# Performance work log

Hardware: AMD Instinct MI355X
Metric: run time of the kernel (lower is better)

Reference implementation:

```python
import jax, jax.numpy as jnp
import numpy as np

B, S, H, NH, HD = 2, 2048, 4096, 32, 128  # batch, seq, hidden, heads, head_dim
THETA = 10000.0
SCALE = HD ** -0.5


def setup_inputs() -> dict:
    key = jax.random.key(0)
    k1, k2, k3 = jax.random.split(key, 3)
    hidden_states = jax.random.normal(k1, (B, S, H), jnp.float32) * 0.02
    w_pack = jax.random.normal(k2, (3 * H, H), jnp.float32) * 0.02  # fused QKV weight
    w_o = jax.random.normal(k3, (H, H), jnp.float32) * 0.02
    positions = jnp.broadcast_to(jnp.arange(S, dtype=jnp.int32), (B, S))
    return {"positions": positions, "hidden_states": hidden_states,
            "w_pack": w_pack, "w_o": w_o}


def _apply_rope(x, positions):
    # x: [B, S, NH, HD]; neox-style (rotate-half) RoPE over full head_dim
    inv_freq = 1.0 / (THETA ** (jnp.arange(0, HD, 2, dtype=jnp.float32) / HD))  # [HD/2]
    ang = positions.astype(jnp.float32)[..., None] * inv_freq  # [B, S, HD/2]
    cos = jnp.cos(ang)[:, :, None, :]  # [B, S, 1, HD/2]
    sin = jnp.sin(ang)[:, :, None, :]
    x1, x2 = x[..., : HD // 2], x[..., HD // 2 :]
    return jnp.concatenate([x1 * cos - x2 * sin, x2 * cos + x1 * sin], axis=-1)


def reference(positions, hidden_states, w_pack, w_o):
    # Fused QKV projection then split (W_pack, bias-free)
    qkv = jnp.einsum('bsh,oh->bso', hidden_states, w_pack)  # [B, S, 3H]
    q, k, v = jnp.split(qkv, 3, axis=-1)
    q = q.reshape(B, S, NH, HD)
    k = k.reshape(B, S, NH, HD)
    v = v.reshape(B, S, NH, HD)
    q = _apply_rope(q, positions)
    k = _apply_rope(k, positions)
    # Causal scaled-dot-product attention
    scores = jnp.einsum('bqhd,bkhd->bhqk', q, k) * SCALE
    causal = jnp.tril(jnp.ones((S, S), dtype=bool))
    scores = jnp.where(causal, scores, jnp.float32(-1e9))
    probs = jax.nn.softmax(scores, axis=-1)
    attn = jnp.einsum('bhqk,bkhd->bqhd', probs, v).reshape(B, S, H)
    return jnp.einsum('bsh,oh->bso', attn, w_o)  # o_proj, bias-free
```

## Files before the change

### kernel.cpp

```cpp
#include <hip/hip_runtime.h>

typedef short short8 __attribute__((ext_vector_type(8)));
typedef float f32x4 __attribute__((ext_vector_type(4)));
typedef unsigned short u16;

static constexpr int BATCH = 2, S = 2048, H = 4096, NHEAD = 32, HDIM = 128;

__device__ __forceinline__ u16 f2b(float f) {
  union { float f; unsigned u; } v; v.f = f;
  return (u16)((v.u + 0x7fffu + ((v.u >> 16) & 1u)) >> 16);
}
__device__ __forceinline__ float b2f(u16 h) {
  union { unsigned u; float f; } v; v.u = ((unsigned)h) << 16;
  return v.f;
}

__device__ __forceinline__ void gl16(const u16* g, u16* l) {
  __builtin_amdgcn_global_load_lds((__attribute__((address_space(1))) void*)g,
                                   (__attribute__((address_space(3))) void*)l,
                                   16, 0, 0);
}

#define MFMA(acc, a, b) \
  acc = __builtin_amdgcn_mfma_f32_16x16x32_bf16(a, b, acc, 0, 0, 0)

__global__ __launch_bounds__(256) void cvt_bf16(const float* __restrict__ in,
                                                u16* __restrict__ out) {
  size_t i = ((size_t)blockIdx.x * 256 + threadIdx.x) * 4;
  float4 v = *(const float4*)(in + i);
  ushort4 o = { f2b(v.x), f2b(v.y), f2b(v.z), f2b(v.w) };
  *(ushort4*)(out + i) = o;
}

template <bool F32OUT>
__global__ __launch_bounds__(512, 2) void gemm256(const u16* __restrict__ A,
                                                  const u16* __restrict__ B,
                                                  void* __restrict__ C,
                                                  int M, int N, int K) {
  __shared__ u16 AL[2][2][128 * 64];
  __shared__ u16 BL[2][2][128 * 64];
  const int nbn = N >> 8;
  const int nwg = (M >> 8) * nbn;
  const int bid = blockIdx.x;
  const int wg = (bid & 7) * (nwg >> 3) + (bid >> 3);
  const int bm = wg / nbn, bn = wg % nbn;
  const int tid = threadIdx.x, lane = tid & 63;
  const int w = tid >> 6, wm = w >> 2, wn = w & 3;
  const int hi = lane >> 4, lo = lane & 15;
  const int nk = K >> 6;

  const u16* Abase = A + (size_t)(bm * 256) * K;
  const u16* Bbase = B + (size_t)(bn * 256) * K;

#define STG_A(buf, half, kt)                                                   \
  { _Pragma("unroll") for (int i = 0; i < 2; ++i) {                            \
      int c = tid + i * 512, r = c >> 3, s = c & 7;                            \
      gl16(Abase + (size_t)((half) * 128 + r) * K + (kt) * 64 +                \
               ((s ^ (r & 7)) * 8),                                            \
           &AL[buf][half][c * 8]);                                             \
    } }
#define STG_B(buf, half, kt)                                                   \
  { _Pragma("unroll") for (int i = 0; i < 2; ++i) {                            \
      int c = tid + i * 512, r = c >> 3, s = c & 7;                            \
      gl16(Bbase + (size_t)((half) * 128 + r) * K + (kt) * 64 +                \
               ((s ^ (r & 7)) * 8),                                            \
           &BL[buf][half][c * 8]);                                             \
    } }
#define PREBAR()                                                               \
  do { __builtin_amdgcn_sched_barrier(0);                                      \
       __builtin_amdgcn_s_barrier(); } while (0)

  f32x4 acc[8][4] = {};

  STG_A(0, 0, 0) STG_A(0, 1, 0) STG_B(0, 0, 0) STG_B(0, 1, 0)
  if (nk > 1) {
    STG_B(1, 0, 1) STG_B(1, 1, 1)
    asm volatile("s_waitcnt vmcnt(4)" ::: "memory");
  } else {
    asm volatile("s_waitcnt vmcnt(0)" ::: "memory");
  }
  __builtin_amdgcn_sched_barrier(0);
  __builtin_amdgcn_s_barrier();

  short8 af[4][2], bf[2][2][2];

  for (int t = 0; t < nk; ++t) {
    const int cur = t & 1;
    const u16* Awave = &AL[cur][wm][0];
    const u16* Bwave = &BL[cur][wn >> 1][0];
    const int lrB = (wn & 1) * 64;

#pragma unroll
    for (int mi = 0; mi < 4; ++mi)
#pragma unroll
      for (int ks = 0; ks < 2; ++ks)
        af[mi][ks] = *(const short8*)&Awave[(mi * 16 + lo) * 64 +
                                            (((ks * 4 + hi) ^ (lo & 7)) * 8)];
#pragma unroll
    for (int ni = 0; ni < 2; ++ni)
#pragma unroll
      for (int ks = 0; ks < 2; ++ks)
        bf[0][ni][ks] = *(const short8*)&Bwave[(lrB + ni * 16 + lo) * 64 +
                                               (((ks * 4 + hi) ^ (lo & 7)) * 8)];
    if (t + 1 < nk) STG_A(cur ^ 1, 0, t + 1)
    PREBAR();
    __builtin_amdgcn_s_setprio(1);
#pragma unroll
    for (int mi = 0; mi < 4; ++mi)
#pragma unroll
      for (int ni = 0; ni < 2; ++ni)
#pragma unroll
        for (int ks = 0; ks < 2; ++ks)
          MFMA(acc[mi][ni], af[mi][ks], bf[0][ni][ks]);
    __builtin_amdgcn_s_setprio(0);
    __builtin_amdgcn_s_barrier();

#pragma unroll
    for (int ni = 0; ni < 2; ++ni)
#pragma unroll
      for (int ks = 0; ks < 2; ++ks)
        bf[1][ni][ks] = *(const short8*)&Bwave[(lrB + 32 + ni * 16 + lo) * 64 +
                                               (((ks * 4 + hi) ^ (lo & 7)) * 8)];
    if (t + 1 < nk) STG_A(cur ^ 1, 1, t + 1)
    PREBAR();
    __builtin_amdgcn_s_setprio(1);
#pragma unroll
    for (int mi = 0; mi < 4; ++mi)
#pragma unroll
      for (int ni = 0; ni < 2; ++ni)
#pragma unroll
        for (int ks = 0; ks < 2; ++ks)
          MFMA(acc[mi][2 + ni], af[mi][ks], bf[1][ni][ks]);
    __builtin_amdgcn_s_setprio(0);
    __builtin_amdgcn_s_barrier();

#pragma unroll
    for (int mi = 0; mi < 4; ++mi)
#pragma unroll
      for (int ks = 0; ks < 2; ++ks)
        af[mi][ks] = *(const short8*)&Awave[((64 + mi * 16 + lo)) * 64 +
                                            (((ks * 4 + hi) ^ (lo & 7)) * 8)];
    if (t + 2 < nk) STG_B(cur, 0, t + 2)
    PREBAR();
    __builtin_amdgcn_s_setprio(1);
#pragma unroll
    for (int mi = 0; mi < 4; ++mi)
#pragma unroll
      for (int ni = 0; ni < 2; ++ni)
#pragma unroll
        for (int ks = 0; ks < 2; ++ks)
          MFMA(acc[4 + mi][2 + ni], af[mi][ks], bf[1][ni][ks]);
    __builtin_amdgcn_s_setprio(0);
    __builtin_amdgcn_s_barrier();

    if (t + 2 < nk) {
      STG_B(cur, 1, t + 2)
      asm volatile("s_waitcnt vmcnt(4)" ::: "memory");
    } else {
      asm volatile("s_waitcnt vmcnt(0)" ::: "memory");
    }
    PREBAR();
    __builtin_amdgcn_s_setprio(1);
#pragma unroll
    for (int mi = 0; mi < 4; ++mi)
#pragma unroll
      for (int ni = 0; ni < 2; ++ni)
#pragma unroll
        for (int ks = 0; ks < 2; ++ks)
          MFMA(acc[4 + mi][ni], af[mi][ks], bf[0][ni][ks]);
    __builtin_amdgcn_s_setprio(0);
    __builtin_amdgcn_s_barrier();
  }

#pragma unroll
  for (int mf = 0; mf < 8; ++mf)
#pragma unroll
    for (int nf = 0; nf < 4; ++nf)
#pragma unroll
      for (int j = 0; j < 4; ++j) {
        size_t idx = (size_t)(bm * 256 + wm * 128 + mf * 16 + hi * 4 + j) * N +
                     bn * 256 + wn * 64 + nf * 16 + lo;
        if (F32OUT) ((float*)C)[idx] = acc[mf][nf][j];
        else        ((u16*)C)[idx]   = f2b(acc[mf][nf][j]);
      }
}

__global__ __launch_bounds__(256) void rope_qk(const u16* __restrict__ qkv,
                                               const int* __restrict__ pos,
                                               u16* __restrict__ qr,
                                               u16* __restrict__ kr) {
  __shared__ float cs[64], sn[64];
  const int bs = blockIdx.x;
  const int b = bs >> 11, s = bs & 2047;
  const int tid = threadIdx.x;
  if (tid < 64) {
    float p = (float)pos[bs];
    float freq = __powf(10000.0f, -(float)tid * (1.0f / 64.0f));
    float a = p * freq;
    sn[tid] = sinf(a);
    cs[tid] = cosf(a);
  }
  __syncthreads();
  const u16* src = qkv + (size_t)bs * 12288;
  for (int i = tid; i < 4096; i += 256) {
    int nh = i >> 7, hd = i & 127, f = hd & 63;
    float c = cs[f], sv = sn[f];
    int oth = (hd < 64) ? i + 64 : i - 64;
    size_t dst = ((size_t)(b * NHEAD + nh) * S + s) * HDIM + hd;
    float x = b2f(src[i]), xo = b2f(src[oth]);
    qr[dst] = f2b((hd < 64) ? (x * c - xo * sv) : (x * c + xo * sv));
    float xk = b2f(src[4096 + i]), xko = b2f(src[4096 + oth]);
    kr[dst] = f2b((hd < 64) ? (xk * c - xko * sv) : (xk * c + xko * sv));
  }
}

__global__ __launch_bounds__(256) void transpose_v(const u16* __restrict__ qkv,
                                                   u16* __restrict__ vt) {
  __shared__ u16 L[64 * 136];
  const int kb = blockIdx.x & 31, bh = blockIdx.x >> 5;
  const int b = bh >> 5, nh = bh & 31;
  const int tid = threadIdx.x;
  const u16* src = qkv + ((size_t)(b * S + kb * 64)) * 12288 + 8192 + nh * 128;
#pragma unroll
  for (int i = 0; i < 4; ++i) {
    int idx = i * 256 + tid, r = idx >> 4, gd = idx & 15;
    *(uint4*)&L[r * 136 + gd * 8] = *(const uint4*)(src + (size_t)r * 12288 + gd * 8);
  }
  __syncthreads();
  u16* dst = vt + ((size_t)bh * S + kb * 64) * 128;
#pragma unroll
  for (int i = 0; i < 4; ++i) {
    int idx = i * 256 + tid;
    int f = idx >> 6, l = idx & 63;
    int ks2 = f >> 3, db = f & 7, hi = l >> 4, lo = l & 15;
    int d = db * 16 + lo;
    int rb = (ks2 * 32 + hi * 8) * 136 + d;
    unsigned e0 = L[rb], e1 = L[rb + 136], e2 = L[rb + 272], e3 = L[rb + 408];
    unsigned e4 = L[rb + 544], e5 = L[rb + 680], e6 = L[rb + 816], e7 = L[rb + 952];
    uint4 o; o.x = e0 | (e1 << 16); o.y = e2 | (e3 << 16);
    o.z = e4 | (e5 << 16); o.w = e6 | (e7 << 16);
    *(uint4*)(dst + (size_t)idx * 8) = o;
  }
}

__global__ __launch_bounds__(256, 2) void flash_fwd(const u16* __restrict__ q,
                                                    const u16* __restrict__ k,
                                                    const u16* __restrict__ vt,
                                                    u16* __restrict__ o) {
  __shared__ u16 KB[2][64 * 128];
  __shared__ u16 VB[2][64 * 128];
  __shared__ u16 Ps[4][16 * 64];
  const int nqt = S / 64;
  const int qt = (nqt - 1) - ((int)blockIdx.x % nqt);
  const int bh = blockIdx.x / nqt;
  const int tid = threadIdx.x, lane = tid & 63, w = tid >> 6;
  const int hi = lane >> 4, lo = lane & 15;

  const u16* qg = q + ((size_t)bh * S + qt * 64 + w * 16) * HDIM;
  short8 qf[4];
#pragma unroll
  for (int ks = 0; ks < 4; ++ks) {
    short8 r = *(const short8*)(qg + (size_t)lo * HDIM + ks * 32 + hi * 8);
    union { short8 s; u16 u[8]; } t; t.s = r;
#pragma unroll
    for (int e = 0; e < 8; ++e)
      t.u[e] = f2b(b2f(t.u[e]) * 0.08838834764831845f);
    qf[ks] = t.s;
  }

  float m_i[4], l_i[4];
  f32x4 oacc[8] = {};
#pragma unroll
  for (int j = 0; j < 4; ++j) { m_i[j] = -1e30f; l_i[j] = 0.0f; }

  const u16* kg = k + (size_t)bh * S * HDIM;
  const u16* vg = vt + (size_t)bh * S * HDIM;

#define STAGE(buf, kvbase)                                                  \
  {                                                                         \
    _Pragma("unroll") for (int i = 0; i < 4; ++i) {                         \
      int idx = i * 256 + tid, r = idx >> 4, gd = idx & 15;                 \
      gl16(kg + (size_t)((kvbase) + r) * HDIM + ((gd ^ (r & 7)) * 8),       \
           &KB[buf][idx * 8]);                                              \
    }                                                                       \
    _Pragma("unroll") for (int i = 0; i < 4; ++i) {                         \
      int idx = i * 256 + tid;                                              \
      gl16(vg + (size_t)(kvbase) * HDIM + idx * 8, &VB[buf][idx * 8]);      \
    }                                                                       \
  }

  STAGE(0, 0)
  int cur = 0;
  u16* PsW = &Ps[w][0];

  for (int kvt = 0; kvt <= qt; ++kvt) {
    if (kvt < qt) {
      STAGE(cur ^ 1, (kvt + 1) * 64)
      asm volatile("s_waitcnt vmcnt(8)" ::: "memory");
    } else {
      asm volatile("s_waitcnt vmcnt(0)" ::: "memory");
    }
    __builtin_amdgcn_s_barrier();
    __builtin_amdgcn_sched_barrier(0);
    const u16* Kc = &KB[cur][0];
    const u16* Vc = &VB[cur][0];

    f32x4 sc[4] = {};
#pragma unroll
    for (int ks = 0; ks < 4; ++ks) {
      const int colu = ks * 32 + hi * 8;
#pragma unroll
      for (int cb = 0; cb < 4; ++cb) {
        const int row = cb * 16 + lo;
        short8 kf = *(const short8*)&Kc[row * 128 + (colu ^ ((row & 7) << 3))];
        MFMA(sc[cb], qf[ks], kf);
      }
    }

    const int qrow = qt * 64 + w * 16 + hi * 4;
    const bool diag = (kvt == qt);
#pragma unroll
    for (int cb = 0; cb < 4; ++cb) {
      const int kvc = kvt * 64 + cb * 16 + lo;
#pragma unroll
      for (int j = 0; j < 4; ++j) {
        float sv = sc[cb][j];
        if (diag && kvc > qrow + j) sv = -1e30f;
        sc[cb][j] = sv;
      }
    }
    float rmax[4], rs[4];
#pragma unroll
    for (int j = 0; j < 4; ++j) {
      rmax[j] = fmaxf(fmaxf(sc[0][j], sc[1][j]), fmaxf(sc[2][j], sc[3][j]));
      for (int d = 8; d; d >>= 1) rmax[j] = fmaxf(rmax[j], __shfl_xor(rmax[j], d));
      float mn = fmaxf(m_i[j], rmax[j]);
      float sf = __expf(m_i[j] - mn);
      m_i[j] = mn; l_i[j] *= sf;
#pragma unroll
      for (int db = 0; db < 8; ++db) oacc[db][j] *= sf;
      rs[j] = 0.0f;
    }
#pragma unroll
    for (int cb = 0; cb < 4; ++cb)
#pragma unroll
      for (int j = 0; j < 4; ++j) {
        float p = __expf(sc[cb][j] - m_i[j]);
        sc[cb][j] = p; rs[j] += p;
      }
#pragma unroll
    for (int j = 0; j < 4; ++j) {
      for (int d = 8; d; d >>= 1) rs[j] += __shfl_xor(rs[j], d);
      l_i[j] += rs[j];
    }

#pragma unroll
    for (int cb = 0; cb < 4; ++cb)
#pragma unroll
      for (int j = 0; j < 4; ++j) {
        const int p = hi * 4 + j;
        PsW[p * 64 + ((cb * 16 + lo) ^ ((p & 7) << 3))] = f2b(sc[cb][j]);
      }
    short8 pf0 = *(const short8*)&PsW[lo * 64 + ((hi * 8) ^ ((lo & 7) << 3))];
    short8 pf1 = *(const short8*)&PsW[lo * 64 + ((32 + hi * 8) ^ ((lo & 7) << 3))];

#pragma unroll
    for (int ks2 = 0; ks2 < 2; ++ks2) {
      const short8 pf = ks2 ? pf1 : pf0;
#pragma unroll
      for (int db = 0; db < 8; ++db) {
        short8 vf = *(const short8*)&Vc[((ks2 * 8 + db) * 64 + lane) * 8];
        MFMA(oacc[db], pf, vf);
      }
    }
    __builtin_amdgcn_s_barrier();
    cur ^= 1;
  }

#pragma unroll
  for (int j = 0; j < 4; ++j) {
    float inv = 1.0f / l_i[j];
    int srow = qt * 64 + w * 16 + hi * 4 + j;
    const int b = bh >> 5, nh = bh & 31;
    size_t base = ((size_t)b * S + srow) * H + (size_t)nh * HDIM + lo;
#pragma unroll
    for (int db = 0; db < 8; ++db)
      o[base + db * 16] = f2b(oacc[db][j] * inv);
  }
}

extern "C" void kernel_launch(void* const* d_in, const int* in_sizes, int n_in,
                              void* d_out, int out_size, void* d_ws, size_t ws_size,
                              hipStream_t stream) {
  const int* pos = (const int*)d_in[0];
  const float* hs = (const float*)d_in[1];
  const float* wpack = (const float*)d_in[2];
  const float* wo = (const float*)d_in[3];
  float* out = (float*)d_out;
  char* ws = (char*)d_ws;
  u16* hs_b    = (u16*)(ws + 0UL);
  u16* wpack_b = (u16*)(ws + 33554432UL);
  u16* wo_b    = (u16*)(ws + 134217728UL);
  u16* qkv_b   = (u16*)(ws + 167772160UL);
  u16* q_r     = (u16*)(ws + 268435456UL);
  u16* k_r     = (u16*)(ws + 301989888UL);
  u16* attn_b  = (u16*)(ws + 335544320UL);
  u16* v_t     = hs_b;

  cvt_bf16<<<16384, 256, 0, stream>>>(hs, hs_b);
  cvt_bf16<<<49152, 256, 0, stream>>>(wpack, wpack_b);
  cvt_bf16<<<16384, 256, 0, stream>>>(wo, wo_b);
  gemm256<false><<<768, 512, 0, stream>>>(hs_b, wpack_b, qkv_b, 4096, 12288, 4096);
  rope_qk<<<4096, 256, 0, stream>>>(qkv_b, pos, q_r, k_r);
  transpose_v<<<2048, 256, 0, stream>>>(qkv_b, v_t);
  flash_fwd<<<64 * 32, 256, 0, stream>>>(q_r, k_r, v_t, attn_b);
  gemm256<true><<<256, 512, 0, stream>>>(attn_b, wo_b, out, 4096, 4096, 4096);
}
```

Before: 965.3 us.

## Fuse RoPE and V transpose into QKV GEMM epilogue via LDS staging

```diff
diff --git a/kernel.cpp b/kernel.cpp
--- a/kernel.cpp
+++ b/kernel.cpp
@@ -32,13 +32,24 @@
   *(ushort4*)(out + i) = o;
 }
 
-template <bool F32OUT>
-__global__ __launch_bounds__(512, 2) void gemm256(const u16* __restrict__ A,
-                                                  const u16* __restrict__ B,
-                                                  void* __restrict__ C,
-                                                  int M, int N, int K) {
-  __shared__ u16 AL[2][2][128 * 64];
-  __shared__ u16 BL[2][2][128 * 64];
+__global__ __launch_bounds__(256) void rope_table(float* __restrict__ tab) {
+  int idx = blockIdx.x * 256 + threadIdx.x;
+  int p = idx >> 6, f = idx & 63;
+  float freq = __powf(10000.0f, -(float)f * (1.0f / 64.0f));
+  float a = (float)p * freq;
+  tab[(size_t)p * 128 + f] = cosf(a);
+  tab[(size_t)p * 128 + 64 + f] = sinf(a);
+}
+
+template <int MODE>
+__global__ __launch_bounds__(512, 2) void gemm256(
+    const u16* __restrict__ A, const u16* __restrict__ B, void* __restrict__ C,
+    int M, int N, int K, const int* __restrict__ pos,
+    const float* __restrict__ tab, u16* __restrict__ qr, u16* __restrict__ kr,
+    u16* __restrict__ vt) {
+  __shared__ u16 SMEM[69632];
+  u16* AL = SMEM;
+  u16* BL = SMEM + 32768;
   const int nbn = N >> 8;
   const int nwg = (M >> 8) * nbn;
   const int bid = blockIdx.x;
@@ -57,14 +68,14 @@
       int c = tid + i * 512, r = c >> 3, s = c & 7;                            \
       gl16(Abase + (size_t)((half) * 128 + r) * K + (kt) * 64 +                \
                ((s ^ (r & 7)) * 8),                                            \
-           &AL[buf][half][c * 8]);                                             \
+           &AL[((buf) * 2 + (half)) * 8192 + c * 8]);                          \
     } }
 #define STG_B(buf, half, kt)                                                   \
   { _Pragma("unroll") for (int i = 0; i < 2; ++i) {                            \
       int c = tid + i * 512, r = c >> 3, s = c & 7;                            \
       gl16(Bbase + (size_t)((half) * 128 + r) * K + (kt) * 64 +                \
                ((s ^ (r & 7)) * 8),                                            \
-           &BL[buf][half][c * 8]);                                             \
+           &BL[((buf) * 2 + (half)) * 8192 + c * 8]);                          \
     } }
 #define PREBAR()                                                               \
   do { __builtin_amdgcn_sched_barrier(0);                                      \
@@ -86,8 +97,8 @@
 
   for (int t = 0; t < nk; ++t) {
     const int cur = t & 1;
-    const u16* Awave = &AL[cur][wm][0];
-    const u16* Bwave = &BL[cur][wn >> 1][0];
+    const u16* Awave = AL + (cur * 2 + wm) * 8192;
+    const u16* Bwave = BL + (cur * 2 + (wn >> 1)) * 8192;
     const int lrB = (wn & 1) * 64;
 
 #pragma unroll
@@ -172,74 +183,82 @@
     __builtin_amdgcn_s_barrier();
   }
 
-#pragma unroll
-  for (int mf = 0; mf < 8; ++mf)
-#pragma unroll
-    for (int nf = 0; nf < 4; ++nf)
-#pragma unroll
-      for (int j = 0; j < 4; ++j) {
-        size_t idx = (size_t)(bm * 256 + wm * 128 + mf * 16 + hi * 4 + j) * N +
-                     bn * 256 + wn * 64 + nf * 16 + lo;
-        if (F32OUT) ((float*)C)[idx] = acc[mf][nf][j];
-        else        ((u16*)C)[idx]   = f2b(acc[mf][nf][j]);
-      }
-}
-
-__global__ __launch_bounds__(256) void rope_qk(const u16* __restrict__ qkv,
-                                               const int* __restrict__ pos,
-                                               u16* __restrict__ qr,
-                                               u16* __restrict__ kr) {
-  __shared__ float cs[64], sn[64];
-  const int bs = blockIdx.x;
-  const int b = bs >> 11, s = bs & 2047;
-  const int tid = threadIdx.x;
-  if (tid < 64) {
-    float p = (float)pos[bs];
-    float freq = __powf(10000.0f, -(float)tid * (1.0f / 64.0f));
-    float a = p * freq;
-    sn[tid] = sinf(a);
-    cs[tid] = cosf(a);
-  }
-  __syncthreads();
-  const u16* src = qkv + (size_t)bs * 12288;
-  for (int i = tid; i < 4096; i += 256) {
-    int nh = i >> 7, hd = i & 127, f = hd & 63;
-    float c = cs[f], sv = sn[f];
-    int oth = (hd < 64) ? i + 64 : i - 64;
-    size_t dst = ((size_t)(b * NHEAD + nh) * S + s) * HDIM + hd;
-    float x = b2f(src[i]), xo = b2f(src[oth]);
-    qr[dst] = f2b((hd < 64) ? (x * c - xo * sv) : (x * c + xo * sv));
-    float xk = b2f(src[4096 + i]), xko = b2f(src[4096 + oth]);
-    kr[dst] = f2b((hd < 64) ? (xk * c - xko * sv) : (xk * c + xko * sv));
-  }
-}
-
-__global__ __launch_bounds__(256) void transpose_v(const u16* __restrict__ qkv,
-                                                   u16* __restrict__ vt) {
-  __shared__ u16 L[64 * 136];
-  const int kb = blockIdx.x & 31, bh = blockIdx.x >> 5;
-  const int b = bh >> 5, nh = bh & 31;
-  const int tid = threadIdx.x;
-  const u16* src = qkv + ((size_t)(b * S + kb * 64)) * 12288 + 8192 + nh * 128;
-#pragma unroll
-  for (int i = 0; i < 4; ++i) {
-    int idx = i * 256 + tid, r = idx >> 4, gd = idx & 15;
-    *(uint4*)&L[r * 136 + gd * 8] = *(const uint4*)(src + (size_t)r * 12288 + gd * 8);
-  }
-  __syncthreads();
-  u16* dst = vt + ((size_t)bh * S + kb * 64) * 128;
-#pragma unroll
-  for (int i = 0; i < 4; ++i) {
-    int idx = i * 256 + tid;
-    int f = idx >> 6, l = idx & 63;
-    int ks2 = f >> 3, db = f & 7, hi = l >> 4, lo = l & 15;
-    int d = db * 16 + lo;
-    int rb = (ks2 * 32 + hi * 8) * 136 + d;
-    unsigned e0 = L[rb], e1 = L[rb + 136], e2 = L[rb + 272], e3 = L[rb + 408];
-    unsigned e4 = L[rb + 544], e5 = L[rb + 680], e6 = L[rb + 816], e7 = L[rb + 952];
-    uint4 o; o.x = e0 | (e1 << 16); o.y = e2 | (e3 << 16);
-    o.z = e4 | (e5 << 16); o.w = e6 | (e7 << 16);
-    *(uint4*)(dst + (size_t)idx * 8) = o;
+  if constexpr (MODE == 1) {
+#pragma unroll
+    for (int mf = 0; mf < 8; ++mf)
+#pragma unroll
+      for (int nf = 0; nf < 4; ++nf)
+#pragma unroll
+        for (int j = 0; j < 4; ++j) {
+          size_t idx = (size_t)(bm * 256 + wm * 128 + mf * 16 + hi * 4 + j) * N +
+                       bn * 256 + wn * 64 + nf * 16 + lo;
+          ((float*)C)[idx] = acc[mf][nf][j];
+        }
+  } else {
+    const int SP = 272;
+    u16* E = SMEM;
+#pragma unroll
+    for (int mf = 0; mf < 8; ++mf)
+#pragma unroll
+      for (int nf = 0; nf < 4; ++nf)
+#pragma unroll
+        for (int j = 0; j < 4; ++j)
+          E[(wm * 128 + mf * 16 + hi * 4 + j) * SP + wn * 64 + nf * 16 + lo] =
+              f2b(acc[mf][nf][j]);
+    __syncthreads();
+
+    const int grow0 = bm * 256, gcol0 = bn * 256;
+    const int bb = grow0 >> 11, s0 = grow0 & 2047;
+    if (gcol0 < 8192) {
+      for (int task = tid; task < 8192; task += 512) {
+        int row = task >> 5, g = task & 31;
+        int gcol = gcol0 + g * 8;
+        int d = gcol & 127, f0 = d & 63;
+        int p = pos[grow0 + row];
+        const float* cp = tab + (size_t)p * 128 + f0;
+        float4 ca = *(const float4*)cp, cb = *(const float4*)(cp + 4);
+        float4 sa = *(const float4*)(cp + 64), sb = *(const float4*)(cp + 68);
+        float cv[8] = {ca.x, ca.y, ca.z, ca.w, cb.x, cb.y, cb.z, cb.w};
+        float sv[8] = {sa.x, sa.y, sa.z, sa.w, sb.x, sb.y, sb.z, sb.w};
+        short8 x = *(const short8*)&E[row * SP + g * 8];
+        short8 xo = *(const short8*)&E[row * SP + (g ^ 8) * 8];
+        float sgn = (d < 64) ? -1.0f : 1.0f;
+        unsigned word[4];
+#pragma unroll
+        for (int pr = 0; pr < 4; ++pr) {
+          float v0 = b2f((u16)x[2 * pr]) * cv[2 * pr] +
+                     sgn * b2f((u16)xo[2 * pr]) * sv[2 * pr];
+          float v1 = b2f((u16)x[2 * pr + 1]) * cv[2 * pr + 1] +
+                     sgn * b2f((u16)xo[2 * pr + 1]) * sv[2 * pr + 1];
+          word[pr] = (unsigned)f2b(v0) | ((unsigned)f2b(v1) << 16);
+        }
+        int hidx = gcol >> 7;
+        u16* outp = (hidx < 32) ? qr : kr;
+        int nh = (hidx < 32) ? hidx : hidx - 32;
+        size_t dst = ((size_t)(bb * 32 + nh) * 2048 + (s0 + row)) * 128 + d;
+        uint4 o = {word[0], word[1], word[2], word[3]};
+        *(uint4*)&outp[dst] = o;
+      }
+    } else {
+      for (int task = tid; task < 8192; task += 512) {
+        int kbl = task >> 11;
+        int hh = (task >> 10) & 1;
+        int c = task & 1023;
+        int f = c >> 6, l = c & 63;
+        int ks2 = f >> 3, db = f & 7, hi2 = l >> 4, lo2 = l & 15;
+        int base = (kbl * 64 + ks2 * 32 + hi2 * 8) * SP + hh * 128 + db * 16 + lo2;
+        unsigned e0 = E[base], e1 = E[base + SP], e2 = E[base + 2 * SP],
+                 e3 = E[base + 3 * SP], e4 = E[base + 4 * SP],
+                 e5 = E[base + 5 * SP], e6 = E[base + 6 * SP],
+                 e7 = E[base + 7 * SP];
+        int nh = ((gcol0 - 8192) >> 7) + hh;
+        size_t dst = ((size_t)(bb * 32 + nh) * 2048 + (s0 + kbl * 64)) * 128 +
+                     (size_t)c * 8;
+        uint4 o = {e0 | (e1 << 16), e2 | (e3 << 16), e4 | (e5 << 16),
+                   e6 | (e7 << 16)};
+        *(uint4*)&vt[dst] = o;
+      }
+    }
   }
 }
 
@@ -401,18 +420,19 @@
   u16* hs_b    = (u16*)(ws + 0UL);
   u16* wpack_b = (u16*)(ws + 33554432UL);
   u16* wo_b    = (u16*)(ws + 134217728UL);
-  u16* qkv_b   = (u16*)(ws + 167772160UL);
+  u16* v_t     = (u16*)(ws + 167772160UL);
+  float* tab   = (float*)(ws + 201326592UL);
   u16* q_r     = (u16*)(ws + 268435456UL);
   u16* k_r     = (u16*)(ws + 301989888UL);
   u16* attn_b  = (u16*)(ws + 335544320UL);
-  u16* v_t     = hs_b;
 
   cvt_bf16<<<16384, 256, 0, stream>>>(hs, hs_b);
   cvt_bf16<<<49152, 256, 0, stream>>>(wpack, wpack_b);
   cvt_bf16<<<16384, 256, 0, stream>>>(wo, wo_b);
-  gemm256<false><<<768, 512, 0, stream>>>(hs_b, wpack_b, qkv_b, 4096, 12288, 4096);
-  rope_qk<<<4096, 256, 0, stream>>>(qkv_b, pos, q_r, k_r);
-  transpose_v<<<2048, 256, 0, stream>>>(qkv_b, v_t);
+  rope_table<<<512, 256, 0, stream>>>(tab);
+  gemm256<0><<<768, 512, 0, stream>>>(hs_b, wpack_b, nullptr, 4096, 12288, 4096,
+                                      pos, tab, q_r, k_r, v_t);
   flash_fwd<<<64 * 32, 256, 0, stream>>>(q_r, k_r, v_t, attn_b);
-  gemm256<true><<<256, 512, 0, stream>>>(attn_b, wo_b, out, 4096, 4096, 4096);
-}
+  gemm256<1><<<256, 512, 0, stream>>>(attn_b, wo_b, out, 4096, 4096, 4096,
+                                      nullptr, nullptr, nullptr, nullptr, nullptr);
+}
```

Measured after the change: 859.0 us. 11.0% less time.
